# Optimization experiments

Measured on AMD Instinct MI355X. Metric: run time of the kernel, lower is better.

Reference implementation:

```python
import jax, jax.numpy as jnp
import numpy as np

NUM_HEADS = 8
ROPE_BASE = 10000.0


def _rope(x):
    # x: [b, n, c]; RoPE with channel_dims=(n,), feature_dim=c, k_max=c//2
    b, n, c = x.shape
    k_max = c // 2
    theta = 1.0 / (ROPE_BASE ** (jnp.arange(k_max, dtype=jnp.float32) / k_max))
    angles = jnp.arange(n, dtype=jnp.float32)[:, None] * theta  # [n, k_max]
    cos = jnp.cos(angles)
    sin = jnp.sin(angles)
    xr = x[..., 0::2]  # real parts  [b, n, k_max]
    xi = x[..., 1::2]  # imag parts
    pr = cos * xr - sin * xi
    pi = cos * xi + sin * xr
    # original concatenates real half then imag half (no re-interleave)
    return jnp.concatenate([pr, pi], axis=-1)


def setup_inputs() -> dict:
    key = jax.random.key(0)
    ks = jax.random.split(key, 5)
    b, n, c = 4, 4096, 1024
    x = jax.random.normal(ks[0], (b, n, c), dtype=jnp.float32)
    qk_w = jax.random.normal(ks[1], (c, 2 * c), dtype=jnp.float32) * (1.0 / np.sqrt(c))
    qk_b = jnp.zeros((2 * c,), dtype=jnp.float32)
    lepe_w = jax.random.normal(ks[2], (3, c, c), dtype=jnp.float32) * (1.0 / np.sqrt(3 * c))  # [W, I, O]
    lepe_b = jnp.zeros((c,), dtype=jnp.float32)
    return {"x": x, "qk_w": qk_w, "qk_b": qk_b, "lepe_w": lepe_w, "lepe_b": lepe_b}


def reference(x, qk_w, qk_b, lepe_w, lepe_b):
    b, n, c = x.shape
    h = NUM_HEADS
    d = c // h

    qk = x @ qk_w + qk_b
    q, k = jnp.split(qk, 2, axis=-1)
    q = jax.nn.elu(q) + 1.0
    k = jax.nn.elu(k) + 1.0

    q_rope = _rope(q)
    k_rope = _rope(k)

    def to_heads(t):  # [b, n, c] -> [b, h, n, d]
        return t.reshape(b, n, h, d).transpose(0, 2, 1, 3)

    qh = to_heads(q)
    kh = to_heads(k)
    qr = to_heads(q_rope)
    kr = to_heads(k_rope)
    vh = to_heads(x)

    # z = 1 / (q . mean_n(k) + eps)  -> [b, h, n, 1]
    k_mean = jnp.mean(kh, axis=2, keepdims=True)  # [b, h, 1, d]
    z = 1.0 / (jnp.einsum('bhnd,bhmd->bhnm', qh, k_mean) + 1e-6)

    # kv = k_rope^T v / sqrt(n)  -> [b, h, d, d]
    kv = jnp.einsum('bhnd,bhne->bhde', kr, vh) * (1.0 / jnp.sqrt(jnp.float32(n)))
    out = jnp.einsum('bhnd,bhde->bhne', qr, kv) * z  # [b, h, n, d]

    out = out.transpose(0, 2, 1, 3).reshape(b, n, c)

    # lepe: Conv1D(dim, 3, padding='same') applied to v (== original x)
    lepe = jax.lax.conv_general_dilated(
        x, lepe_w, window_strides=(1,), padding='SAME',
        dimension_numbers=('NWC', 'WIO', 'NWC')) + lepe_b
    return out + lepe
```

## Files before the change

kernel.cpp:

```cpp
#include <hip/hip_runtime.h>
#include <cmath>

#define BB 4
#define NN 4096
#define CC 1024
#define HH 8
#define DD 128
#define MM (BB*NN)
#define NP (NN+2)

typedef __attribute__((ext_vector_type(8))) short bf16x8;
typedef __attribute__((ext_vector_type(4))) float f32x4;

static __device__ __forceinline__ unsigned short f2bf(float f) {
    unsigned int u = __float_as_uint(f);
    unsigned int r = (u + 0x7FFF + ((u >> 16) & 1)) >> 16;
    return (unsigned short)r;
}
static __device__ __forceinline__ float bf2f(short s) {
    return __uint_as_float(((unsigned int)(unsigned short)s) << 16);
}
static __device__ __forceinline__ float4 bf4(ushort4 u) {
    float4 f;
    f.x = __uint_as_float((unsigned int)u.x << 16);
    f.y = __uint_as_float((unsigned int)u.y << 16);
    f.z = __uint_as_float((unsigned int)u.z << 16);
    f.w = __uint_as_float((unsigned int)u.w << 16);
    return f;
}

static __device__ __forceinline__ void load_lds16(const void* g, void* l) {
    __builtin_amdgcn_global_load_lds(
        (const __attribute__((address_space(1))) unsigned int*)g,
        (__attribute__((address_space(3))) unsigned int*)l, 16, 0, 0);
}

static __device__ __forceinline__ int swz(int row, int ko) {
    return (row * 64 + ko) ^ ((row & 7) << 3);
}

#define CFENCE() asm volatile("" ::: "memory")

__global__ __launch_bounds__(256) void padx_kernel(
    const float* __restrict__ x, unsigned short* __restrict__ xpad)
{
    const int r = blockIdx.x;
    const int b = r / NP, p = r % NP;
    const int c = threadIdx.x * 4;
    ushort4 v = {0, 0, 0, 0};
    if (p >= 1 && p <= NN) {
        const float4 f = *(const float4*)&x[(size_t)(b * NN + p - 1) * CC + c];
        v.x = f2bf(f.x); v.y = f2bf(f.y); v.z = f2bf(f.z); v.w = f2bf(f.w);
    }
    *(ushort4*)&xpad[(size_t)r * CC + c] = v;
}

__global__ __launch_bounds__(256) void transpose_bf16_kernel(
    const float* __restrict__ src, unsigned short* __restrict__ dst,
    int R, int Cc)
{
    __shared__ float t[32][33];
    const int r0 = blockIdx.y * 32, c0 = blockIdx.x * 32;
    const int tx = threadIdx.x & 31, ty = threadIdx.x >> 5;
    #pragma unroll
    for (int i = 0; i < 4; ++i) {
        int r = ty + i * 8;
        t[r][tx] = src[(size_t)(r0 + r) * Cc + c0 + tx];
    }
    __syncthreads();
    #pragma unroll
    for (int i = 0; i < 4; ++i) {
        int r = ty + i * 8;
        dst[(size_t)(c0 + r) * R + r0 + tx] = f2bf(t[tx][r]);
    }
}

static __device__ __forceinline__ void stage_tile(
    const unsigned short* __restrict__ g, int stride,
    unsigned short* lds, int tid)
{
    const int wb = tid & ~63;
    #pragma unroll
    for (int l = 0; l < 4; ++l) {
        const int c = l * 512 + tid;
        const int row = c >> 3;
        const int col8 = (c & 7) ^ (row & 7);
        load_lds16(&g[(size_t)row * stride + col8 * 8],
                   &lds[(size_t)(l * 512 + wb) * 8]);
    }
}
static __device__ __forceinline__ void stage_ab(
    const unsigned short* __restrict__ Ag, int astride,
    const unsigned short* __restrict__ Bg, int bstride,
    unsigned short* As, unsigned short* Bs, int tid)
{
    stage_tile(Ag, astride, As, tid);
    stage_tile(Bg, bstride, Bs, tid);
}

static __device__ __forceinline__ void mfma_tile(
    const unsigned short* __restrict__ Ab, const unsigned short* __restrict__ Bb,
    int wr, int wc, int lane, f32x4 acc[8][4])
{
    const int rl = lane & 15;
    __builtin_amdgcn_s_setprio(1);
    #pragma unroll
    for (int ks = 0; ks < 2; ++ks) {
        const int ko = ks * 32 + (lane >> 4) * 8;
        bf16x8 af[8], bfr[4];
        #pragma unroll
        for (int mf = 0; mf < 8; ++mf)
            af[mf] = *(const bf16x8*)&Ab[swz(wr * 128 + mf * 16 + rl, ko)];
        #pragma unroll
        for (int nf = 0; nf < 4; ++nf)
            bfr[nf] = *(const bf16x8*)&Bb[swz(wc * 64 + nf * 16 + rl, ko)];
        #pragma unroll
        for (int mf = 0; mf < 8; ++mf)
            #pragma unroll
            for (int nf = 0; nf < 4; ++nf)
                acc[mf][nf] = __builtin_amdgcn_mfma_f32_16x16x32_bf16(
                    af[mf], bfr[nf], acc[mf][nf], 0, 0, 0);
    }
    __builtin_amdgcn_s_setprio(0);
}

__global__ __launch_bounds__(512) void gemm_qk_mfma(
    const unsigned short* __restrict__ xpad, const unsigned short* __restrict__ wT,
    const float* __restrict__ bias, unsigned short* __restrict__ qbuf,
    unsigned short* __restrict__ kbuf, float* __restrict__ ksum)
{
    __shared__ __align__(16) unsigned short As[2][16384];
    __shared__ __align__(16) unsigned short Bs[2][16384];
    const int m0 = blockIdx.x * 256;
    const int n0 = blockIdx.y * 256;
    const int tid = threadIdx.x;
    const int lane = tid & 63;
    const int wv = tid >> 6;
    const int wr = wv >> 2, wc = wv & 3;
    const int b = m0 >> 12;
    const int rbase = m0 + 1 + 2 * b;

    f32x4 acc[8][4] = {};
    stage_ab(&xpad[(size_t)rbase * CC], CC, &wT[(size_t)n0 * CC], CC,
             As[0], Bs[0], tid);
    for (int kt = 0; kt < 16; ++kt) {
        const int cur = kt & 1;
        if (kt + 1 < 16) {
            stage_ab(&xpad[(size_t)rbase * CC + (kt + 1) * 64], CC,
                     &wT[(size_t)n0 * CC + (kt + 1) * 64], CC,
                     As[cur ^ 1], Bs[cur ^ 1], tid);
            asm volatile("s_waitcnt vmcnt(8)" ::: "memory");
        } else {
            asm volatile("s_waitcnt vmcnt(0)" ::: "memory");
        }
        __builtin_amdgcn_s_barrier();
        CFENCE();
        mfma_tile(As[cur], Bs[cur], wr, wc, lane, acc);
        CFENCE();
        __builtin_amdgcn_s_barrier();
    }
    const bool khalf = (n0 >= CC);
    const int col = lane & 15, rb4 = (lane >> 4) * 4;
    #pragma unroll
    for (int nf = 0; nf < 4; ++nf) {
        const int n = n0 + wc * 64 + nf * 16 + col;
        const float bn = bias[n];
        float csum = 0.0f;
        #pragma unroll
        for (int mf = 0; mf < 8; ++mf)
            #pragma unroll
            for (int r = 0; r < 4; ++r) {
                const int m = m0 + wr * 128 + mf * 16 + rb4 + r;
                float v = acc[mf][nf][r] + bn;
                v = (v > 0.0f) ? (v + 1.0f) : __expf(v);
                csum += v;
                if (!khalf) qbuf[(size_t)m * CC + n] = f2bf(v);
                else        kbuf[(size_t)m * CC + (n - CC)] = f2bf(v);
            }
        if (khalf) atomicAdd(&ksum[b * CC + (n - CC)], csum);
    }
}

__global__ __launch_bounds__(256) void rope_z_kernel(
    unsigned short* __restrict__ qbuf, const unsigned short* __restrict__ kbuf,
    const float* __restrict__ ksum, unsigned short* __restrict__ krP,
    float* __restrict__ zbuf)
{
    const int tid = threadIdx.x;
    const int row = tid >> 3;
    const int h = tid & 7;
    const int m = blockIdx.x * 32 + row;
    const int b = m >> 12;
    const int pos = m & (NN - 1);
    unsigned short* qrow = qbuf + (size_t)m * CC + h * DD;
    const unsigned short* krow = kbuf + (size_t)m * CC + h * DD;

    bf16x8 qv[16], kv8[16];
    #pragma unroll
    for (int i = 0; i < 16; ++i) {
        qv[i]  = *(const bf16x8*)&qrow[i * 8];
        kv8[i] = *(const bf16x8*)&krow[i * 8];
    }
    const float* km = ksum + b * CC + h * DD;
    float dot = 0.0f;
    #pragma unroll
    for (int i = 0; i < 16; ++i)
        #pragma unroll
        for (int jq = 0; jq < 8; ++jq)
            dot = fmaf(bf2f(qv[i][jq]), km[i * 8 + jq], dot);
    dot *= (1.0f / (float)NN);
    __syncthreads();
    zbuf[(size_t)m * HH + h] = 1.0f / (dot + 1e-6f);

    #pragma unroll
    for (int c8 = 0; c8 < 8; ++c8) {
        bf16x8 qpr, qpi, kpr, kpi;
        #pragma unroll
        for (int u = 0; u < 8; ++u) {
            const int jj = c8 * 8 + u;
            const int j = h * 64 + jj;
            const float theta = __builtin_exp2f((float)j * (-13.287712379549449f / 512.0f));
            float sv, cv;
            __sincosf((float)pos * theta, &sv, &cv);
            const int li = c8 * 2 + (u >> 2);
            const int le = (2 * u) & 7;
            const float q0 = bf2f(qv[li][le]),  q1 = bf2f(qv[li][le + 1]);
            const float k0 = bf2f(kv8[li][le]), k1 = bf2f(kv8[li][le + 1]);
            qpr[u] = (short)f2bf(cv * q0 - sv * q1);
            qpi[u] = (short)f2bf(cv * q1 + sv * q0);
            kpr[u] = (short)f2bf(cv * k0 - sv * k1);
            kpi[u] = (short)f2bf(cv * k1 + sv * k0);
        }
        *(bf16x8*)&qbuf[(size_t)m * CC + h * 64 + c8 * 8] = qpr;
        *(bf16x8*)&qbuf[(size_t)m * CC + 512 + h * 64 + c8 * 8] = qpi;
        unsigned short* kp1 = &krP[((size_t)(b * 8 + (h >> 1)) * NN + pos) * DD + (h & 1) * 64 + c8 * 8];
        unsigned short* kp2 = &krP[((size_t)(b * 8 + 4 + (h >> 1)) * NN + pos) * DD + (h & 1) * 64 + c8 * 8];
        *(bf16x8*)kp1 = kpr;
        *(bf16x8*)kp2 = kpi;
    }
}

__global__ __launch_bounds__(256) void kv_kernel(
    const unsigned short* __restrict__ krP, const unsigned short* __restrict__ xpad,
    float* __restrict__ kvpart)
{
    __shared__ float ksm[8][132];
    __shared__ float vsm[8][132];
    const int bh = blockIdx.x;
    const int slice = blockIdx.y;
    const int b = bh >> 3, h = bh & 7;
    const int n0 = slice * 256;
    const int tid = threadIdx.x;
    const int td = (tid >> 4) * 8;
    const int te = (tid & 15) * 8;
    const unsigned short* kp = krP + ((size_t)bh * NN + n0) * DD;
    const unsigned short* vp = xpad + ((size_t)(b * NP) + 1 + n0) * CC + h * DD;
    const int sr = tid >> 5;
    const int sc = (tid & 31) * 4;
    float acc[8][8] = {};
    ushort4 kq = *(const ushort4*)&kp[(size_t)sr * DD + sc];
    ushort4 vq = *(const ushort4*)&vp[(size_t)sr * CC + sc];
    for (int r0 = 0; r0 < 256; r0 += 8) {
        *(float4*)&ksm[sr][sc] = bf4(kq);
        *(float4*)&vsm[sr][sc] = bf4(vq);
        __syncthreads();
        if (r0 + 8 < 256) {
            kq = *(const ushort4*)&kp[(size_t)(r0 + 8 + sr) * DD + sc];
            vq = *(const ushort4*)&vp[(size_t)(r0 + 8 + sr) * CC + sc];
        }
        #pragma unroll
        for (int r = 0; r < 8; ++r) {
            float a[8], bv[8];
            *(float4*)&a[0]  = *(const float4*)&ksm[r][td];
            *(float4*)&a[4]  = *(const float4*)&ksm[r][td + 4];
            *(float4*)&bv[0] = *(const float4*)&vsm[r][te];
            *(float4*)&bv[4] = *(const float4*)&vsm[r][te + 4];
            #pragma unroll
            for (int i = 0; i < 8; ++i)
                #pragma unroll
                for (int j = 0; j < 8; ++j)
                    acc[i][j] = fmaf(a[i], bv[j], acc[i][j]);
        }
        __syncthreads();
    }
    float* op = kvpart + ((size_t)slice * 32 + bh) * (DD * DD);
    #pragma unroll
    for (int i = 0; i < 8; ++i)
        #pragma unroll
        for (int j = 0; j < 8; j += 4)
            *(float4*)&op[(td + i) * DD + te + j] = *(float4*)&acc[i][j];
}

__global__ __launch_bounds__(256) void kv_reduce_t_kernel(
    const float* __restrict__ kvpart, unsigned short* __restrict__ kvT)
{
    __shared__ float t[32][33];
    const int bh = blockIdx.y;
    const int dblk = blockIdx.x >> 2, eblk = blockIdx.x & 3;
    const int tx = threadIdx.x & 31, ty = threadIdx.x >> 5;
    #pragma unroll
    for (int i = 0; i < 4; ++i) {
        const int d = dblk * 32 + ty + i * 8;
        float s = 0.0f;
        #pragma unroll
        for (int sl = 0; sl < 16; ++sl)
            s += kvpart[((size_t)sl * 32 + bh) * (DD * DD) + (size_t)d * DD + eblk * 32 + tx];
        t[ty + i * 8][tx] = s * (1.0f / 64.0f);
    }
    __syncthreads();
    #pragma unroll
    for (int i = 0; i < 4; ++i) {
        const int e = ty + i * 8;
        kvT[((size_t)bh * DD + eblk * 32 + e) * DD + dblk * 32 + tx] = f2bf(t[tx][e]);
    }
}

__global__ __launch_bounds__(512) void lepe_mfma(
    const unsigned short* __restrict__ xpad, const unsigned short* __restrict__ wT,
    const float* __restrict__ bias, const unsigned short* __restrict__ qr,
    const unsigned short* __restrict__ kvT, const float* __restrict__ z,
    float* __restrict__ out)
{
    __shared__ __align__(16) unsigned short As[2][16384];
    __shared__ __align__(16) unsigned short Bs[2][16384];
    const int m0 = blockIdx.x * 256;
    const int n0 = blockIdx.y * 256;
    const int tid = threadIdx.x;
    const int lane = tid & 63;
    const int wv = tid >> 6;
    const int wr = wv >> 2, wc = wv & 3;
    const int b = m0 >> 12;
    const int rbase = m0 + 1 + 2 * b;
    const int rb4 = (lane >> 4) * 4;
    const int h0 = n0 >> 7;
    const int hw = h0 + (wc >> 1);

    f32x4 acc[8][4] = {};

    #pragma unroll
    for (int kt = 0; kt < 2; ++kt) {
        stage_tile(&qr[(size_t)m0 * CC + h0 * DD + kt * 64], CC, As[0], tid);
        stage_tile(&qr[(size_t)m0 * CC + (h0 + 1) * DD + kt * 64], CC, As[1], tid);
        stage_tile(&kvT[(size_t)(b * 8 + h0) * DD * DD + kt * 64], DD, Bs[0], tid);
        __syncthreads();
        mfma_tile(As[wc >> 1], Bs[0], wr, wc, lane, acc);
        __syncthreads();
    }

    #pragma unroll
    for (int mf = 0; mf < 8; ++mf)
        #pragma unroll
        for (int r = 0; r < 4; ++r) {
            const float zz = z[(size_t)(m0 + wr * 128 + mf * 16 + rb4 + r) * HH + hw];
            #pragma unroll
            for (int nf = 0; nf < 4; ++nf)
                acc[mf][nf][r] *= zz;
        }
    asm volatile("s_waitcnt vmcnt(0)" ::: "memory");

    stage_ab(&xpad[(size_t)(rbase - 1) * CC], CC, &wT[(size_t)n0 * (3 * CC)], 3 * CC,
             As[0], Bs[0], tid);
    for (int kt = 0; kt < 48; ++kt) {
        const int cur = kt & 1;
        if (kt + 1 < 48) {
            const int k0n = (kt + 1) * 64;
            const int sh = (k0n >> 10) - 1;
            const int i0 = k0n & (CC - 1);
            stage_ab(&xpad[(size_t)(rbase + sh) * CC + i0], CC,
                     &wT[(size_t)n0 * (3 * CC) + k0n], 3 * CC,
                     As[cur ^ 1], Bs[cur ^ 1], tid);
            asm volatile("s_waitcnt vmcnt(8)" ::: "memory");
        } else {
            asm volatile("s_waitcnt vmcnt(0)" ::: "memory");
        }
        __builtin_amdgcn_s_barrier();
        CFENCE();
        mfma_tile(As[cur], Bs[cur], wr, wc, lane, acc);
        CFENCE();
        __builtin_amdgcn_s_barrier();
    }

    const int col = lane & 15;
    #pragma unroll
    for (int nf = 0; nf < 4; ++nf) {
        const int n = n0 + wc * 64 + nf * 16 + col;
        const float bn = bias[n];
        #pragma unroll
        for (int mf = 0; mf < 8; ++mf)
            #pragma unroll
            for (int r = 0; r < 4; ++r) {
                const int m = m0 + wr * 128 + mf * 16 + rb4 + r;
                out[(size_t)m * CC + n] = acc[mf][nf][r] + bn;
            }
    }
}

extern "C" void kernel_launch(void* const* d_in, const int* in_sizes, int n_in,
                              void* d_out, int out_size, void* d_ws, size_t ws_size,
                              hipStream_t stream)
{
    const float* x      = (const float*)d_in[0];
    const float* qk_w   = (const float*)d_in[1];
    const float* qk_b   = (const float*)d_in[2];
    const float* lepe_w = (const float*)d_in[3];
    const float* lepe_b = (const float*)d_in[4];
    float* out = (float*)d_out;

    float* ws     = (float*)d_ws;
    float* zbuf   = ws;
    float* ksum   = zbuf + (size_t)MM * HH;
    float* kvpart = ksum + (size_t)BB * CC;
    unsigned short* xpad = (unsigned short*)(kvpart + (size_t)16 * 32 * DD * DD);
    unsigned short* wqT  = xpad + (size_t)BB * NP * CC;
    unsigned short* wlT  = wqT + (size_t)2 * CC * CC;
    unsigned short* qbuf = wlT + (size_t)CC * 3 * CC;
    unsigned short* kbuf = qbuf + (size_t)MM * CC;
    unsigned short* krP  = kbuf + (size_t)MM * CC;
    unsigned short* kvT  = krP + (size_t)32 * NN * DD;

    hipMemsetAsync(ksum, 0, BB * CC * sizeof(float), stream);

    padx_kernel          <<<BB * NP,                      256, 0, stream>>>(x, xpad);
    transpose_bf16_kernel<<<dim3(2 * CC / 32, CC / 32),   256, 0, stream>>>(qk_w, wqT, CC, 2 * CC);
    transpose_bf16_kernel<<<dim3(CC / 32, 3 * CC / 32),   256, 0, stream>>>(lepe_w, wlT, 3 * CC, CC);

    gemm_qk_mfma      <<<dim3(MM / 256, 2048 / 256), 512, 0, stream>>>(xpad, wqT, qk_b, qbuf, kbuf, ksum);
    rope_z_kernel     <<<MM / 32,                    256, 0, stream>>>(qbuf, kbuf, ksum, krP, zbuf);
    kv_kernel         <<<dim3(32, 16),               256, 0, stream>>>(krP, xpad, kvpart);
    kv_reduce_t_kernel<<<dim3(16, 32),               256, 0, stream>>>(kvpart, kvT);
    lepe_mfma         <<<dim3(MM / 256, CC / 256),   512, 0, stream>>>(xpad, wlT, lepe_b, qbuf, kvT, zbuf, out);
}
```

Measured before the change: 510.5 us.

## Split GEMM k-tiles into four interleaved phases of LDS reads, MFMA and staging

The main loops of the QK projection GEMM and the fused lepe GEMM are restructured into a four-phase schedule. Each phase loads a quarter of the fragments from LDS, issues 16 MFMAs, and starts one half-tile global-to-LDS prefetch, with barriers between phases. The aim is to spread memory traffic across the MFMA work and lower register pressure by holding only 4 A fragments at a time. In exchange it adds many more barriers per k-tile and uses finer-grained vmcnt waits, which could cost synchronization overhead.

After: 521.0 us. 1.02x slower.

```diff
diff --git a/kernel.cpp b/kernel.cpp
--- a/kernel.cpp
+++ b/kernel.cpp
@@ -40,6 +40,7 @@
 }
 
 #define CFENCE() asm volatile("" ::: "memory")
+#define BAR() do { CFENCE(); __builtin_amdgcn_s_barrier(); CFENCE(); } while (0)
 
 __global__ __launch_bounds__(256) void padx_kernel(
     const float* __restrict__ x, unsigned short* __restrict__ xpad)
@@ -75,13 +76,13 @@
     }
 }
 
-static __device__ __forceinline__ void stage_tile(
+static __device__ __forceinline__ void stage_half(
     const unsigned short* __restrict__ g, int stride,
     unsigned short* lds, int tid)
 {
     const int wb = tid & ~63;
     #pragma unroll
-    for (int l = 0; l < 4; ++l) {
+    for (int l = 0; l < 2; ++l) {
         const int c = l * 512 + tid;
         const int row = c >> 3;
         const int col8 = (c & 7) ^ (row & 7);
@@ -89,48 +90,71 @@
                    &lds[(size_t)(l * 512 + wb) * 8]);
     }
 }
-static __device__ __forceinline__ void stage_ab(
-    const unsigned short* __restrict__ Ag, int astride,
-    const unsigned short* __restrict__ Bg, int bstride,
-    unsigned short* As, unsigned short* Bs, int tid)
-{
-    stage_tile(Ag, astride, As, tid);
-    stage_tile(Bg, bstride, Bs, tid);
-}
-
-static __device__ __forceinline__ void mfma_tile(
-    const unsigned short* __restrict__ Ab, const unsigned short* __restrict__ Bb,
-    int wr, int wc, int lane, f32x4 acc[8][4])
-{
-    const int rl = lane & 15;
+
+static __device__ __forceinline__ void lda4(
+    const unsigned short* __restrict__ h, int lr0, int rl, int ko, bf16x8* o)
+{
+    #pragma unroll
+    for (int i = 0; i < 4; ++i)
+        o[i] = *(const bf16x8*)&h[swz(lr0 + i * 16 + rl, ko)];
+}
+
+static __device__ __forceinline__ void mfma_quad(
+    f32x4 (*acc)[4], int mfb, const bf16x8* af, const bf16x8* bfr)
+{
     __builtin_amdgcn_s_setprio(1);
     #pragma unroll
-    for (int ks = 0; ks < 2; ++ks) {
-        const int ko = ks * 32 + (lane >> 4) * 8;
-        bf16x8 af[8], bfr[4];
-        #pragma unroll
-        for (int mf = 0; mf < 8; ++mf)
-            af[mf] = *(const bf16x8*)&Ab[swz(wr * 128 + mf * 16 + rl, ko)];
+    for (int i = 0; i < 4; ++i)
         #pragma unroll
         for (int nf = 0; nf < 4; ++nf)
-            bfr[nf] = *(const bf16x8*)&Bb[swz(wc * 64 + nf * 16 + rl, ko)];
-        #pragma unroll
-        for (int mf = 0; mf < 8; ++mf)
-            #pragma unroll
-            for (int nf = 0; nf < 4; ++nf)
-                acc[mf][nf] = __builtin_amdgcn_mfma_f32_16x16x32_bf16(
-                    af[mf], bfr[nf], acc[mf][nf], 0, 0, 0);
-    }
+            acc[mfb + i][nf] = __builtin_amdgcn_mfma_f32_16x16x32_bf16(
+                af[i], bfr[nf], acc[mfb + i][nf], 0, 0, 0);
     __builtin_amdgcn_s_setprio(0);
 }
+
+#define KTILE_4PHASE(Ah, Bh, blr0, STAGE_A0, STAGE_A1, STAGE_B0, STAGE_B1, HAVE_NEXT) \
+    do {                                                                     \
+        bf16x8 af_[4], af2_[4], bfr_[4], bfr2_[4];                           \
+                                                                \
+        if (HAVE_NEXT) {                                                     \
+            STAGE_A0;                                                        \
+            asm volatile("s_waitcnt vmcnt(2)" ::: "memory");                 \
+        } else {                                                             \
+            asm volatile("s_waitcnt vmcnt(0)" ::: "memory");                 \
+        }                                                                    \
+        BAR();                                                               \
+        lda4(Ah, 0, rl, ko0, af_);                                           \
+        lda4(Bh, blr0, rl, ko0, bfr_);                                       \
+        mfma_quad(acc, 0, af_, bfr_);                                        \
+        BAR();                                                               \
+                                                                \
+        lda4(Ah, 64, rl, ko0, af2_);                                         \
+        if (HAVE_NEXT) { STAGE_A1; }                                         \
+        BAR();                                                               \
+        mfma_quad(acc, 4, af2_, bfr_);                                       \
+        BAR();                                                               \
+                                                                \
+        lda4(Ah, 0, rl, ko1, af_);                                           \
+        lda4(Bh, blr0, rl, ko1, bfr2_);                                      \
+        if (HAVE_NEXT) { STAGE_B0; }                                         \
+        BAR();                                                               \
+        mfma_quad(acc, 0, af_, bfr2_);                                       \
+        BAR();                                                               \
+                                                                \
+        lda4(Ah, 64, rl, ko1, af2_);                                         \
+        if (HAVE_NEXT) { STAGE_B1; }                                         \
+        BAR();                                                               \
+        mfma_quad(acc, 4, af2_, bfr2_);                                      \
+        BAR();                                                               \
+    } while (0)
 
 __global__ __launch_bounds__(512) void gemm_qk_mfma(
     const unsigned short* __restrict__ xpad, const unsigned short* __restrict__ wT,
     const float* __restrict__ bias, unsigned short* __restrict__ qbuf,
     unsigned short* __restrict__ kbuf, float* __restrict__ ksum)
 {
-    __shared__ __align__(16) unsigned short As[2][16384];
-    __shared__ __align__(16) unsigned short Bs[2][16384];
+    __shared__ __align__(16) unsigned short SA[2][2][8192];
+    __shared__ __align__(16) unsigned short SB[2][2][8192];
     const int m0 = blockIdx.x * 256;
     const int n0 = blockIdx.y * 256;
     const int tid = threadIdx.x;
@@ -139,26 +163,34 @@
     const int wr = wv >> 2, wc = wv & 3;
     const int b = m0 >> 12;
     const int rbase = m0 + 1 + 2 * b;
+    const int rl = lane & 15;
+    const int ko0 = (lane >> 4) * 8;
+    const int ko1 = 32 + ko0;
+    const int blr0 = (wc & 1) * 64;
+
+    const unsigned short* Agl = &xpad[(size_t)rbase * CC];
+    const unsigned short* Bgl = &wT[(size_t)n0 * CC];
 
     f32x4 acc[8][4] = {};
-    stage_ab(&xpad[(size_t)rbase * CC], CC, &wT[(size_t)n0 * CC], CC,
-             As[0], Bs[0], tid);
-    for (int kt = 0; kt < 16; ++kt) {
-        const int cur = kt & 1;
-        if (kt + 1 < 16) {
-            stage_ab(&xpad[(size_t)rbase * CC + (kt + 1) * 64], CC,
-                     &wT[(size_t)n0 * CC + (kt + 1) * 64], CC,
-                     As[cur ^ 1], Bs[cur ^ 1], tid);
-            asm volatile("s_waitcnt vmcnt(8)" ::: "memory");
-        } else {
-            asm volatile("s_waitcnt vmcnt(0)" ::: "memory");
-        }
-        __builtin_amdgcn_s_barrier();
-        CFENCE();
-        mfma_tile(As[cur], Bs[cur], wr, wc, lane, acc);
-        CFENCE();
-        __builtin_amdgcn_s_barrier();
-    }
+    stage_half(Agl, CC, SA[0][0], tid);
+    stage_half(&Agl[(size_t)128 * CC], CC, SA[0][1], tid);
+    stage_half(Bgl, CC, SB[0][0], tid);
+    stage_half(&Bgl[(size_t)128 * CC], CC, SB[0][1], tid);
+
+    const int NT = 16;
+    for (int t = 0; t < NT; ++t) {
+        const int cur = t & 1;
+        const unsigned short* Ah = SA[cur][wr];
+        const unsigned short* Bh = SB[cur][wc >> 1];
+        const int k1 = (t + 1) * 64;
+        KTILE_4PHASE(Ah, Bh, blr0,
+            stage_half(&Agl[k1], CC, SA[cur ^ 1][0], tid),
+            stage_half(&Agl[(size_t)128 * CC + k1], CC, SA[cur ^ 1][1], tid),
+            stage_half(&Bgl[k1], CC, SB[cur ^ 1][0], tid),
+            stage_half(&Bgl[(size_t)128 * CC + k1], CC, SB[cur ^ 1][1], tid),
+            (t + 1 < NT));
+    }
+
     const bool khalf = (n0 >= CC);
     const int col = lane & 15, rb4 = (lane >> 4) * 4;
     #pragma unroll
@@ -321,8 +353,8 @@
     const unsigned short* __restrict__ kvT, const float* __restrict__ z,
     float* __restrict__ out)
 {
-    __shared__ __align__(16) unsigned short As[2][16384];
-    __shared__ __align__(16) unsigned short Bs[2][16384];
+    __shared__ __align__(16) unsigned short SA[2][2][8192];
+    __shared__ __align__(16) unsigned short SB[2][2][8192];
     const int m0 = blockIdx.x * 256;
     const int n0 = blockIdx.y * 256;
     const int tid = threadIdx.x;
@@ -331,6 +363,10 @@
     const int wr = wv >> 2, wc = wv & 3;
     const int b = m0 >> 12;
     const int rbase = m0 + 1 + 2 * b;
+    const int rl = lane & 15;
+    const int ko0 = (lane >> 4) * 8;
+    const int ko1 = 32 + ko0;
+    const int blr0 = (wc & 1) * 64;
     const int rb4 = (lane >> 4) * 4;
     const int h0 = n0 >> 7;
     const int hw = h0 + (wc >> 1);
@@ -339,11 +375,26 @@
 
     #pragma unroll
     for (int kt = 0; kt < 2; ++kt) {
-        stage_tile(&qr[(size_t)m0 * CC + h0 * DD + kt * 64], CC, As[0], tid);
-        stage_tile(&qr[(size_t)m0 * CC + (h0 + 1) * DD + kt * 64], CC, As[1], tid);
-        stage_tile(&kvT[(size_t)(b * 8 + h0) * DD * DD + kt * 64], DD, Bs[0], tid);
+        stage_half(&qr[(size_t)m0 * CC + h0 * DD + kt * 64], CC, SA[0][0], tid);
+        stage_half(&qr[(size_t)(m0 + 128) * CC + h0 * DD + kt * 64], CC, SA[0][1], tid);
+        stage_half(&qr[(size_t)m0 * CC + (h0 + 1) * DD + kt * 64], CC, SA[1][0], tid);
+        stage_half(&qr[(size_t)(m0 + 128) * CC + (h0 + 1) * DD + kt * 64], CC, SA[1][1], tid);
+        stage_half(&kvT[(size_t)(b * 8 + h0) * DD * DD + kt * 64], DD, SB[0][0], tid);
+        stage_half(&kvT[(size_t)(b * 8 + h0) * DD * DD + (size_t)128 * DD + kt * 64], DD, SB[0][1], tid);
         __syncthreads();
-        mfma_tile(As[wc >> 1], Bs[0], wr, wc, lane, acc);
+        const unsigned short* Ah = SA[wc >> 1][wr];
+        const unsigned short* Bh = SB[0][wc >> 1];
+        bf16x8 af[4], af2[4], bfr[4], bfr2[4];
+        lda4(Ah, 0, rl, ko0, af);
+        lda4(Bh, blr0, rl, ko0, bfr);
+        mfma_quad(acc, 0, af, bfr);
+        lda4(Ah, 64, rl, ko0, af2);
+        mfma_quad(acc, 4, af2, bfr);
+        lda4(Ah, 0, rl, ko1, af);
+        lda4(Bh, blr0, rl, ko1, bfr2);
+        mfma_quad(acc, 0, af, bfr2);
+        lda4(Ah, 64, rl, ko1, af2);
+        mfma_quad(acc, 4, af2, bfr2);
         __syncthreads();
     }
 
@@ -358,26 +409,29 @@
         }
     asm volatile("s_waitcnt vmcnt(0)" ::: "memory");
 
-    stage_ab(&xpad[(size_t)(rbase - 1) * CC], CC, &wT[(size_t)n0 * (3 * CC)], 3 * CC,
-             As[0], Bs[0], tid);
-    for (int kt = 0; kt < 48; ++kt) {
-        const int cur = kt & 1;
-        if (kt + 1 < 48) {
-            const int k0n = (kt + 1) * 64;
-            const int sh = (k0n >> 10) - 1;
-            const int i0 = k0n & (CC - 1);
-            stage_ab(&xpad[(size_t)(rbase + sh) * CC + i0], CC,
-                     &wT[(size_t)n0 * (3 * CC) + k0n], 3 * CC,
-                     As[cur ^ 1], Bs[cur ^ 1], tid);
-            asm volatile("s_waitcnt vmcnt(8)" ::: "memory");
-        } else {
-            asm volatile("s_waitcnt vmcnt(0)" ::: "memory");
-        }
-        __builtin_amdgcn_s_barrier();
-        CFENCE();
-        mfma_tile(As[cur], Bs[cur], wr, wc, lane, acc);
-        CFENCE();
-        __builtin_amdgcn_s_barrier();
+    const unsigned short* Bgl = &wT[(size_t)n0 * (3 * CC)];
+    {
+        const unsigned short* A0 = &xpad[(size_t)(rbase - 1) * CC];
+        stage_half(A0, CC, SA[0][0], tid);
+        stage_half(&A0[(size_t)128 * CC], CC, SA[0][1], tid);
+        stage_half(Bgl, 3 * CC, SB[0][0], tid);
+        stage_half(&Bgl[(size_t)128 * (3 * CC)], 3 * CC, SB[0][1], tid);
+    }
+    const int NT = 48;
+    for (int t = 0; t < NT; ++t) {
+        const int cur = t & 1;
+        const unsigned short* Ah = SA[cur][wr];
+        const unsigned short* Bh = SB[cur][wc >> 1];
+        const int k1 = (t + 1) * 64;
+        const int sh1 = (k1 >> 10) - 1;
+        const int i1 = k1 & (CC - 1);
+        const unsigned short* An = &xpad[(size_t)(rbase + sh1) * CC + i1];
+        KTILE_4PHASE(Ah, Bh, blr0,
+            stage_half(An, CC, SA[cur ^ 1][0], tid),
+            stage_half(&An[(size_t)128 * CC], CC, SA[cur ^ 1][1], tid),
+            stage_half(&Bgl[k1], 3 * CC, SB[cur ^ 1][0], tid),
+            stage_half(&Bgl[(size_t)128 * (3 * CC) + k1], 3 * CC, SB[cur ^ 1][1], tid),
+            (t + 1 < NT));
     }
 
     const int col = lane & 15;
```
